# Kernel tuning notes

Measured on AMD Instinct MI355X. Metric: run time of the kernel, lower is better.

The kernel has to match this reference:

```python
import jax, jax.numpy as jnp
import numpy as np

CONF_THRESH = 0.3
NMS_THRESH = 0.5
TOP_K = 64
VAR = (0.1, 0.2)  # standard SSD decode variances


def setup_inputs() -> dict:
    key = jax.random.key(0)
    k1, k2, k3 = jax.random.split(key, 3)
    B, A, C = 16, 16384, 81
    loc = jax.random.normal(k1, (B, A, 4), jnp.float32)
    conf = jax.random.normal(k2, (B, A, C), jnp.float32)
    anchors = jax.random.uniform(k3, (A, 4), jnp.float32)  # cxcywh in [0,1]
    return {"loc": loc, "conf": conf, "anchors": anchors}


def _decode(loc, anchors):
    # SSD-style decode: loc [A,4] offsets, anchors [A,4] cxcywh -> corners [A,4]
    cxcy = anchors[:, :2] + loc[:, :2] * VAR[0] * anchors[:, 2:]
    wh = anchors[:, 2:] * jnp.exp(loc[:, 2:] * VAR[1])
    tl = cxcy - wh * 0.5
    return jnp.concatenate([tl, tl + wh], axis=1)


def _iou(box, boxes):
    # box [4], boxes [A,4] in corner format
    tl = jnp.maximum(box[:2], boxes[:, :2])
    br = jnp.minimum(box[2:], boxes[:, 2:])
    wh = jnp.clip(br - tl, 0.0)
    inter = wh[:, 0] * wh[:, 1]
    a1 = (box[2] - box[0]) * (box[3] - box[1])
    a2 = (boxes[:, 2] - boxes[:, 0]) * (boxes[:, 3] - boxes[:, 1])
    return inter / (a1 + a2 - inter)


def _nms(boxes, scores):
    # greedy NMS for one (batch, class) lane; boxes [A,4], scores [A]
    s0 = jnp.where(scores > CONF_THRESH, scores, -1.0)

    def step(s, _):
        i = jnp.argmax(s)
        sc = s[i]
        box = boxes[i]
        keep = sc > 0.0  # -1 means masked/suppressed; valid scores > conf_thresh > 0
        supp = jnp.where(_iou(box, boxes) > NMS_THRESH, -1.0, s).at[i].set(-1.0)
        s_next = jnp.where(keep, supp, s)
        row = jnp.where(keep, jnp.concatenate([sc[None], box]),
                        jnp.zeros((5,), s.dtype))
        return s_next, row

    _, rows = jax.lax.scan(step, s0, None, length=TOP_K)
    return rows  # [TOP_K, 5] = (score, x1, y1, x2, y2), zero-padded


def reference(loc, conf, anchors):
    conf = jax.nn.sigmoid(conf)                      # [B,A,C]
    boxes = jax.vmap(_decode, in_axes=(0, None))(loc, anchors)  # [B,A,4]
    scores = jnp.swapaxes(conf, 1, 2)                # [B,C,A]
    per_class = jax.vmap(_nms, in_axes=(None, 0))    # over classes
    out = jax.vmap(per_class)(boxes, scores)         # [B,C,TOP_K,5]
    return out
```

## Files before the change

### kernel.cpp

```cpp
#include <hip/hip_runtime.h>
#include <math.h>

constexpr int B_N  = 16;
constexpr int A_N  = 16384;
constexpr int C_N  = 81;
constexpr int TOPK = 64;
constexpr int DNT  = 256;
constexpr int NBINS = 232;
constexpr int CAP   = 512;
constexpr unsigned BIN_BASE = 0x3E99u;
constexpr int SNT = 256;
constexpr int BC_N = B_N * C_N;

constexpr int TA   = 64;
constexpr int TNT  = 256;
constexpr int TILE_ELEMS = TA * C_N;
constexpr int TILE_F4    = TILE_ELEMS / 4;

__global__ __launch_bounds__(DNT) void decode_kernel(const float4* __restrict__ loc,
                                                     const float4* __restrict__ anch,
                                                     float4* __restrict__ boxes) {
    int i = blockIdx.x * DNT + threadIdx.x;
    int a = i & (A_N - 1);
    float4 l  = loc[i];
    float4 an = anch[a];
    float cx = an.x + (l.x * 0.1f) * an.z;
    float cy = an.y + (l.y * 0.1f) * an.w;
    float w  = an.z * expf(l.z * 0.2f);
    float h  = an.w * expf(l.w * 0.2f);
    float x1 = cx - w * 0.5f;
    float y1 = cy - h * 0.5f;
    boxes[i] = make_float4(x1, y1, x1 + w, y1 + h);
}

__global__ __launch_bounds__(TNT) void sigT_kernel(const float* __restrict__ conf,
                                                   float* __restrict__ scoresT) {
    __shared__ float4 tile4[TILE_F4];
    float* tile = (float*)tile4;

    const int a0 = blockIdx.x * TA;
    const int b  = blockIdx.y;
    const int t  = threadIdx.x;

    const float4* src = (const float4*)(conf + ((size_t)b * A_N + a0) * C_N);
#pragma unroll
    for (int i = 0; i < (TILE_F4 + TNT - 1) / TNT; ++i) {
        int idx4 = i * TNT + t;
        if (idx4 < TILE_F4) {
            float4 x = src[idx4];
            float4 v;
            v.x = 1.0f / (1.0f + expf(-x.x));
            v.y = 1.0f / (1.0f + expf(-x.y));
            v.z = 1.0f / (1.0f + expf(-x.z));
            v.w = 1.0f / (1.0f + expf(-x.w));
            tile4[idx4] = v;
        }
    }
    __syncthreads();
    float* dst = scoresT + (size_t)b * C_N * A_N + a0;
#pragma unroll
    for (int i = 0; i < (TILE_F4 + TNT - 1) / TNT; ++i) {
        int idx4 = i * TNT + t;
        if (idx4 < TILE_F4) {
            int cc  = idx4 >> 4;
            int al4 = idx4 & 15;
            int e   = al4 * 4 * C_N + cc;
            float4 v;
            v.x = tile[e];
            v.y = tile[e + C_N];
            v.z = tile[e + 2 * C_N];
            v.w = tile[e + 3 * C_N];
            ((float4*)(dst + (size_t)cc * A_N))[al4] = v;
        }
    }
}

__device__ __forceinline__ void sort_gather_scan64(
        unsigned long long* cand, float4* cbox, int C, int lane,
        const float4* __restrict__ bptr, float* __restrict__ optr,
        float& rx1, float& ry1, float& rx2, float& ry2, float& rar,
        int& acc, int& kout) {
    unsigned long long key[8];
#pragma unroll
    for (int r = 0; r < 8; ++r) {
        int sidx = r * 64 + lane;
        key[r] = (sidx < C) ? cand[sidx] : 0ull;
    }
#pragma unroll
    for (int k = 2; k <= CAP; k <<= 1) {
#pragma unroll
        for (int j = k >> 1; j > 0; j >>= 1) {
            if (j >= 64) {
                int jr = j >> 6;
#pragma unroll
                for (int r = 0; r < 8; ++r) {
                    int rp = r ^ jr;
                    if (rp > r) {
                        int e = r * 64 + lane;
                        bool up = ((e & k) == 0);
                        unsigned long long va = key[r], vb = key[rp];
                        bool sw = up ? (va < vb) : (va > vb);
                        if (sw) { key[r] = vb; key[rp] = va; }
                    }
                }
            } else {
#pragma unroll
                for (int r = 0; r < 8; ++r) {
                    int e = r * 64 + lane;
                    bool up    = ((e & k) == 0);
                    bool isLow = ((lane & j) == 0);
                    unsigned long long va = key[r];
                    unsigned long long vb = __shfl_xor(va, j, 64);
                    bool keepMax = (up == isLow);
                    key[r] = keepMax ? (va > vb ? va : vb) : (va < vb ? va : vb);
                }
            }
        }
    }
    __syncthreads();
#pragma unroll
    for (int r = 0; r < 8; ++r) cand[r * 64 + lane] = key[r];
    __syncthreads();
#pragma unroll
    for (int r = 0; r < 8; ++r) {
        int e = r * 64 + lane;
        if (e < C) cbox[e] = bptr[(int)(~(unsigned)cand[e])];
    }
    __syncthreads();

    int ts = 0;
    unsigned long long k0 = cand[0];
    float4 cb = cbox[0];
    while (ts < C) {
        unsigned long long nk = 0ull;
        float4 nb = cb;
        if (ts + 1 < C) { nk = cand[ts + 1]; nb = cbox[ts + 1]; }
        float sc = __uint_as_float((unsigned)(k0 >> 32));
        float ca = (cb.z - cb.x) * (cb.w - cb.y);
        bool over = false;
        if (lane < acc) {
            float tlx = fmaxf(rx1, cb.x);
            float tly = fmaxf(ry1, cb.y);
            float brx = fminf(rx2, cb.z);
            float bry = fminf(ry2, cb.w);
            float iw  = fmaxf(brx - tlx, 0.0f);
            float ih  = fmaxf(bry - tly, 0.0f);
            float inter = iw * ih;
            float iou = inter / (rar + ca - inter);
            over = iou > 0.5f;
        }
        if (!__any(over)) {
            if (lane == acc) { rx1 = cb.x; ry1 = cb.y; rx2 = cb.z; ry2 = cb.w; rar = ca; }
            if (lane == 0) {
                float* o = optr + (size_t)kout * 5;
                o[0] = sc; o[1] = cb.x; o[2] = cb.y; o[3] = cb.z; o[4] = cb.w;
            }
            acc++; kout++;
            if (acc == TOPK) break;
        }
        ++ts; k0 = nk; cb = nb;
    }
}

__global__ __launch_bounds__(SNT) void select_kernel(
        const float* __restrict__ scoresT,
        unsigned long long* __restrict__ g_cand,
        int* __restrict__ g_hist,
        int* __restrict__ g_cnt,
        int* __restrict__ g_blo) {
    __shared__ int hist[NBINS];
    __shared__ int s_cnt;

    const int bc = blockIdx.x;
    const int t  = threadIdx.x;

    for (int i = t; i < NBINS; i += SNT) hist[i] = 0;
    if (t == 0) s_cnt = 0;
    __syncthreads();

    const float4* sptr = (const float4*)(scoresT + (size_t)bc * A_N);

    for (int i = 0; i < A_N / 4 / SNT; ++i) {
        float4 s4 = sptr[t + SNT * i];
        float s[4] = {s4.x, s4.y, s4.z, s4.w};
#pragma unroll
        for (int q = 0; q < 4; ++q) {
            if (s[q] > 0.3f) {
                unsigned u = __float_as_uint(s[q]);
                int bin = (int)(u >> 16) - (int)BIN_BASE;
                bin = bin < 0 ? 0 : (bin > NBINS - 1 ? NBINS - 1 : bin);
                atomicAdd(&hist[bin], 1);
            }
        }
    }
    __syncthreads();

    for (int i = t; i < NBINS; i += SNT) g_hist[bc * NBINS + i] = hist[i];

    int lo = NBINS, tot = 0;
    while (lo > 0) {
        int cnt = hist[lo - 1];
        if (tot + cnt > CAP) {
            if (tot == 0) { lo--; }
            break;
        }
        tot += cnt; lo--;
    }
    const int bin_lo = lo;

    if (bin_lo < NBINS) {
        for (int i = 0; i < A_N / 4 / SNT; ++i) {
            float4 s4 = sptr[t + SNT * i];
            float s[4] = {s4.x, s4.y, s4.z, s4.w};
#pragma unroll
            for (int q = 0; q < 4; ++q) {
                if (s[q] > 0.3f) {
                    unsigned u = __float_as_uint(s[q]);
                    int bin = (int)(u >> 16) - (int)BIN_BASE;
                    bin = bin < 0 ? 0 : (bin > NBINS - 1 ? NBINS - 1 : bin);
                    if (bin >= bin_lo && bin < NBINS) {
                        int slot = atomicAdd(&s_cnt, 1);
                        if (slot < CAP) {
                            unsigned a = (unsigned)(4 * (t + SNT * i) + q);
                            g_cand[(size_t)bc * CAP + slot] =
                                ((unsigned long long)u << 32) | (unsigned)(~a);
                        }
                    }
                }
            }
        }
    }
    __syncthreads();
    if (t == 0) {
        int C = s_cnt; if (C > CAP) C = CAP;
        g_cnt[bc] = C;
        g_blo[bc] = bin_lo;
    }
}

__global__ __launch_bounds__(64, 4) void nms_sorted_kernel(
        const float* __restrict__ scoresT,
        const float4* __restrict__ boxes,
        const unsigned long long* __restrict__ g_cand,
        const int* __restrict__ g_hist,
        const int* __restrict__ g_cnt,
        const int* __restrict__ g_blo,
        float* __restrict__ out) {
    __shared__ int hist[NBINS];
    __shared__ unsigned long long cand[CAP];
    __shared__ float4 cbox[CAP];
    __shared__ int s_cnt;

    const int bc   = blockIdx.x;
    const int b    = bc / C_N;
    const int lane = threadIdx.x;

    const float4* sptr = (const float4*)(scoresT + (size_t)bc * A_N);
    const float4* bptr = boxes + (size_t)b * A_N;
    float* optr = out + (size_t)bc * TOPK * 5;

    for (int i = lane; i < NBINS; i += 64) hist[i] = g_hist[bc * NBINS + i];
    const int C0 = g_cnt[bc];
    int bin_hi   = g_blo[bc];
    for (int e = lane; e < C0; e += 64) cand[e] = g_cand[(size_t)bc * CAP + e];
    __syncthreads();

    float rx1 = 0.f, ry1 = 0.f, rx2 = 0.f, ry2 = 0.f, rar = 0.f;
    int acc = 0, kout = 0;

    if (C0 > 0)
        sort_gather_scan64(cand, cbox, C0, lane, bptr, optr,
                           rx1, ry1, rx2, ry2, rar, acc, kout);

    while (acc < TOPK) {
        int lo = bin_hi, tot = 0;
        while (lo > 0) {
            int cnt = hist[lo - 1];
            if (tot + cnt > CAP) {
                if (tot == 0) { lo--; }
                break;
            }
            tot += cnt; lo--;
        }
        const int bin_lo = lo;
        if (bin_lo == bin_hi) break;
        if (lane == 0) s_cnt = 0;
        __syncthreads();

        for (int i = 0; i < A_N / 4 / 64; ++i) {
            float4 s4 = sptr[lane + 64 * i];
            float s[4] = {s4.x, s4.y, s4.z, s4.w};
#pragma unroll
            for (int q = 0; q < 4; ++q) {
                if (s[q] > 0.3f) {
                    unsigned u = __float_as_uint(s[q]);
                    int bin = (int)(u >> 16) - (int)BIN_BASE;
                    bin = bin < 0 ? 0 : (bin > NBINS - 1 ? NBINS - 1 : bin);
                    if (bin >= bin_lo && bin < bin_hi) {
                        int slot = atomicAdd(&s_cnt, 1);
                        if (slot < CAP) {
                            unsigned a = (unsigned)(4 * (lane + 64 * i) + q);
                            cand[slot] = ((unsigned long long)u << 32) | (unsigned)(~a);
                        }
                    }
                }
            }
        }
        __syncthreads();
        int C = s_cnt; if (C > CAP) C = CAP;
        if (C > 0)
            sort_gather_scan64(cand, cbox, C, lane, bptr, optr,
                               rx1, ry1, rx2, ry2, rar, acc, kout);
        bin_hi = bin_lo;
    }

    {
        float* o  = optr + (size_t)kout * 5;
        int   rem = (TOPK - kout) * 5;
        for (int i = lane; i < rem; i += 64) o[i] = 0.0f;
    }
}

__global__ __launch_bounds__(SNT, 4) void select_nms_fused(
        const float* __restrict__ scoresT,
        const float4* __restrict__ boxes,
        float* __restrict__ out) {
    __shared__ int hist[NBINS];
    __shared__ unsigned long long cand[CAP];
    __shared__ float4 cbox[CAP];
    __shared__ int s_cnt, s_acc, s_kout;

    const int bc   = blockIdx.x;
    const int b    = bc / C_N;
    const int t    = threadIdx.x;
    const int lane = t & 63;
    const int wv   = t >> 6;

    for (int i = t; i < NBINS; i += SNT) hist[i] = 0;
    if (t == 0) { s_acc = 0; s_kout = 0; }
    __syncthreads();

    const float4* sptr = (const float4*)(scoresT + (size_t)bc * A_N);
    const float4* bptr = boxes + (size_t)b * A_N;
    float* optr = out + (size_t)bc * TOPK * 5;

    for (int i = 0; i < A_N / 4 / SNT; ++i) {
        float4 s4 = sptr[t + SNT * i];
        float s[4] = {s4.x, s4.y, s4.z, s4.w};
#pragma unroll
        for (int q = 0; q < 4; ++q) {
            if (s[q] > 0.3f) {
                unsigned u = __float_as_uint(s[q]);
                int bin = (int)(u >> 16) - (int)BIN_BASE;
                bin = bin < 0 ? 0 : (bin > NBINS - 1 ? NBINS - 1 : bin);
                atomicAdd(&hist[bin], 1);
            }
        }
    }
    __syncthreads();

    float rx1 = 0.f, ry1 = 0.f, rx2 = 0.f, ry2 = 0.f, rar = 0.f;
    int acc = 0, kout = 0;

    int bin_hi = NBINS;
    for (;;) {
        int lo = bin_hi, tot = 0;
        while (lo > 0) {
            int cnt = hist[lo - 1];
            if (tot + cnt > CAP) { if (tot == 0) { lo--; } break; }
            tot += cnt; lo--;
        }
        const int bin_lo = lo;
        if (bin_lo == bin_hi) break;
        if (t == 0) s_cnt = 0;
        __syncthreads();

        for (int i = 0; i < A_N / 4 / SNT; ++i) {
            float4 s4 = sptr[t + SNT * i];
            float s[4] = {s4.x, s4.y, s4.z, s4.w};
#pragma unroll
            for (int q = 0; q < 4; ++q) {
                if (s[q] > 0.3f) {
                    unsigned u = __float_as_uint(s[q]);
                    int bin = (int)(u >> 16) - (int)BIN_BASE;
                    bin = bin < 0 ? 0 : (bin > NBINS - 1 ? NBINS - 1 : bin);
                    if (bin >= bin_lo && bin < bin_hi) {
                        int slot = atomicAdd(&s_cnt, 1);
                        if (slot < CAP) {
                            unsigned a = (unsigned)(4 * (t + SNT * i) + q);
                            cand[slot] = ((unsigned long long)u << 32) | (unsigned)(~a);
                        }
                    }
                }
            }
        }
        __syncthreads();
        int C = s_cnt; if (C > CAP) C = CAP;

        if (C > 0) {
            if (wv == 0) {
                unsigned long long key[8];
#pragma unroll
                for (int r = 0; r < 8; ++r) {
                    int sidx = r * 64 + lane;
                    key[r] = (sidx < C) ? cand[sidx] : 0ull;
                }
#pragma unroll
                for (int k = 2; k <= CAP; k <<= 1) {
#pragma unroll
                    for (int j = k >> 1; j > 0; j >>= 1) {
                        if (j >= 64) {
                            int jr = j >> 6;
#pragma unroll
                            for (int r = 0; r < 8; ++r) {
                                int rp = r ^ jr;
                                if (rp > r) {
                                    int e = r * 64 + lane;
                                    bool up = ((e & k) == 0);
                                    unsigned long long va = key[r], vb = key[rp];
                                    bool sw = up ? (va < vb) : (va > vb);
                                    if (sw) { key[r] = vb; key[rp] = va; }
                                }
                            }
                        } else {
#pragma unroll
                            for (int r = 0; r < 8; ++r) {
                                int e = r * 64 + lane;
                                bool up    = ((e & k) == 0);
                                bool isLow = ((lane & j) == 0);
                                unsigned long long va = key[r];
                                unsigned long long vb = __shfl_xor(va, j, 64);
                                bool keepMax = (up == isLow);
                                key[r] = keepMax ? (va > vb ? va : vb)
                                                 : (va < vb ? va : vb);
                            }
                        }
                    }
                }
#pragma unroll
                for (int r = 0; r < 8; ++r) cand[r * 64 + lane] = key[r];
            }
            __syncthreads();

            for (int e = t; e < CAP; e += SNT)
                if (e < C) cbox[e] = bptr[(int)(~(unsigned)cand[e])];
            __syncthreads();

            if (wv == 0) {
                int ts = 0;
                unsigned long long k0 = cand[0];
                float4 cb = cbox[0];
                while (ts < C) {
                    unsigned long long nk = 0ull;
                    float4 nb = cb;
                    if (ts + 1 < C) { nk = cand[ts + 1]; nb = cbox[ts + 1]; }
                    float sc = __uint_as_float((unsigned)(k0 >> 32));
                    float ca = (cb.z - cb.x) * (cb.w - cb.y);
                    bool over = false;
                    if (lane < acc) {
                        float tlx = fmaxf(rx1, cb.x);
                        float tly = fmaxf(ry1, cb.y);
                        float brx = fminf(rx2, cb.z);
                        float bry = fminf(ry2, cb.w);
                        float iw  = fmaxf(brx - tlx, 0.0f);
                        float ih  = fmaxf(bry - tly, 0.0f);
                        float inter = iw * ih;
                        float iou = inter / (rar + ca - inter);
                        over = iou > 0.5f;
                    }
                    if (!__any(over)) {
                        if (lane == acc) { rx1 = cb.x; ry1 = cb.y; rx2 = cb.z; ry2 = cb.w; rar = ca; }
                        if (lane == 0) {
                            float* o = optr + (size_t)kout * 5;
                            o[0] = sc; o[1] = cb.x; o[2] = cb.y; o[3] = cb.z; o[4] = cb.w;
                        }
                        acc++; kout++;
                        if (acc == TOPK) break;
                    }
                    ++ts; k0 = nk; cb = nb;
                }
                if (lane == 0) { s_acc = acc; s_kout = kout; }
            }
            __syncthreads();
            if (s_acc >= TOPK) break;
        }
        bin_hi = bin_lo;
    }

    {
        const int ko = s_kout;
        float* o  = optr + (size_t)ko * 5;
        int   rem = (TOPK - ko) * 5;
        for (int i = t; i < rem; i += SNT) o[i] = 0.0f;
    }
}

__global__ __launch_bounds__(64, 4) void nms_fallback(const float* __restrict__ conf,
                                                      const float4* __restrict__ boxes,
                                                      float* __restrict__ out) {
    __shared__ int hist[NBINS];
    __shared__ unsigned long long cand[CAP];
    __shared__ float4 cbox[CAP];
    __shared__ int s_cnt;

    const int c    = blockIdx.x;
    const int b    = blockIdx.y;
    const int lane = threadIdx.x;

    const float4* bptr = boxes + (size_t)b * A_N;
    const float*  cptr = conf + (size_t)b * A_N * C_N + c;
    float* optr = out + (size_t)(b * C_N + c) * TOPK * 5;

    for (int i = lane; i < NBINS; i += 64) hist[i] = 0;
    __syncthreads();
    for (int i = 0; i < A_N / 256; ++i) {
        int a0 = 4 * (lane + 64 * i);
#pragma unroll
        for (int q = 0; q < 4; ++q) {
            float x = cptr[(size_t)(a0 + q) * C_N];
            float s = 1.0f / (1.0f + expf(-x));
            if (s > 0.3f) {
                unsigned u = __float_as_uint(s);
                int bin = (int)(u >> 16) - (int)BIN_BASE;
                bin = bin < 0 ? 0 : (bin > NBINS - 1 ? NBINS - 1 : bin);
                atomicAdd(&hist[bin], 1);
            }
        }
    }
    __syncthreads();

    float rx1 = 0.f, ry1 = 0.f, rx2 = 0.f, ry2 = 0.f, rar = 0.f;
    int acc = 0, kout = 0;
    int bin_hi = NBINS;
    for (;;) {
        int lo = bin_hi, tot = 0;
        while (lo > 0) {
            int cnt = hist[lo - 1];
            if (tot + cnt > CAP) { if (tot == 0) { lo--; } break; }
            tot += cnt; lo--;
        }
        const int bin_lo = lo;
        if (bin_lo == bin_hi) break;
        if (lane == 0) s_cnt = 0;
        __syncthreads();
        for (int i = 0; i < A_N / 256; ++i) {
            int a0 = 4 * (lane + 64 * i);
#pragma unroll
            for (int q = 0; q < 4; ++q) {
                float x = cptr[(size_t)(a0 + q) * C_N];
                float s = 1.0f / (1.0f + expf(-x));
                if (s > 0.3f) {
                    unsigned u = __float_as_uint(s);
                    int bin = (int)(u >> 16) - (int)BIN_BASE;
                    bin = bin < 0 ? 0 : (bin > NBINS - 1 ? NBINS - 1 : bin);
                    if (bin >= bin_lo && bin < bin_hi) {
                        int slot = atomicAdd(&s_cnt, 1);
                        if (slot < CAP)
                            cand[slot] = ((unsigned long long)u << 32) | (unsigned)(~(unsigned)(a0 + q));
                    }
                }
            }
        }
        __syncthreads();
        int C = s_cnt; if (C > CAP) C = CAP;
        if (C > 0)
            sort_gather_scan64(cand, cbox, C, lane, bptr, optr,
                               rx1, ry1, rx2, ry2, rar, acc, kout);
        if (acc == TOPK) break;
        bin_hi = bin_lo;
    }
    {
        float* o  = optr + (size_t)kout * 5;
        int   rem = (TOPK - kout) * 5;
        for (int i = lane; i < rem; i += 64) o[i] = 0.0f;
    }
}

extern "C" void kernel_launch(void* const* d_in, const int* in_sizes, int n_in,
                              void* d_out, int out_size, void* d_ws, size_t ws_size,
                              hipStream_t stream) {
    const float* loc     = (const float*)d_in[0];
    const float* conf    = (const float*)d_in[1];
    const float* anchors = (const float*)d_in[2];
    float* out = (float*)d_out;

    const size_t boxes_bytes  = (size_t)B_N * A_N * sizeof(float4);
    const size_t scores_bytes = (size_t)B_N * C_N * A_N * sizeof(float);
    const size_t cand_bytes   = (size_t)BC_N * CAP * sizeof(unsigned long long);
    const size_t hist_bytes   = (size_t)BC_N * NBINS * sizeof(int);
    const size_t cnt_bytes    = (size_t)BC_N * sizeof(int);
    const size_t full_bytes   = boxes_bytes + scores_bytes + cand_bytes +
                                hist_bytes + 2 * cnt_bytes;

    float4* boxes = (float4*)d_ws;

    decode_kernel<<<(B_N * A_N) / DNT, DNT, 0, stream>>>(
        (const float4*)loc, (const float4*)anchors, boxes);

    if (ws_size >= full_bytes) {
        char* p = (char*)d_ws + boxes_bytes;
        float* scoresT = (float*)p;                 p += scores_bytes;
        unsigned long long* g_cand = (unsigned long long*)p; p += cand_bytes;
        int* g_hist = (int*)p;                      p += hist_bytes;
        int* g_cnt  = (int*)p;                      p += cnt_bytes;
        int* g_blo  = (int*)p;

        sigT_kernel<<<dim3(A_N / TA, B_N), TNT, 0, stream>>>(conf, scoresT);
        select_kernel<<<dim3(BC_N), SNT, 0, stream>>>(scoresT, g_cand, g_hist, g_cnt, g_blo);
        nms_sorted_kernel<<<dim3(BC_N), 64, 0, stream>>>(scoresT, boxes, g_cand,
                                                         g_hist, g_cnt, g_blo, out);
    } else if (ws_size >= boxes_bytes + scores_bytes) {
        float* scoresT = (float*)((char*)d_ws + boxes_bytes);
        sigT_kernel<<<dim3(A_N / TA, B_N), TNT, 0, stream>>>(conf, scoresT);
        select_nms_fused<<<dim3(BC_N), SNT, 0, stream>>>(scoresT, boxes, out);
    } else {
        nms_fallback<<<dim3(C_N, B_N), 64, 0, stream>>>(conf, boxes, out);
    }
}
```

Measured before the change: 221.7 us.

## Replace sequential candidate scan with register bitonic sort and parallel suppression

Adds process_band64, which sorts each band of up to 512 candidates with a register-resident bitonic network using wave shuffles. It then does greedy NMS by having each accepted box suppress all register-held candidates in parallel through an alive bitmask and ballot. This replaces the earlier scan, which tested every candidate against the accepted boxes one at a time (one lane per accepted box, with __any). Accepted boxes are kept in shared memory so later bands can be pre-suppressed. It costs more registers, so launch bounds drop from 4 to 2 blocks per SM.

```diff
diff --git a/kernel.cpp b/kernel.cpp
--- a/kernel.cpp
+++ b/kernel.cpp
@@ -162,6 +162,118 @@
     }
 }
 
+__device__ __forceinline__ void suppress_pass(
+        unsigned& aliveM, const float4& bb, float bar,
+        const float4 (&breg)[8], const float (&careg)[8]) {
+#pragma unroll
+    for (int r = 0; r < 8; ++r) {
+        float tlx = fmaxf(bb.x, breg[r].x);
+        float tly = fmaxf(bb.y, breg[r].y);
+        float brx = fminf(bb.z, breg[r].z);
+        float bry = fminf(bb.w, breg[r].w);
+        float iw  = fmaxf(brx - tlx, 0.0f);
+        float ih  = fmaxf(bry - tly, 0.0f);
+        float inter = iw * ih;
+        float iou = inter / (bar + careg[r] - inter);
+        if (iou > 0.5f) aliveM &= ~(1u << r);
+    }
+}
+
+__device__ __forceinline__ void process_band64(
+        unsigned long long* cand, float4* cbox, float4* abox, float* aar,
+        int C, int lane,
+        const float4* __restrict__ bptr, float* __restrict__ optr,
+        int& acc, int& kout) {
+    unsigned long long key[8];
+#pragma unroll
+    for (int r = 0; r < 8; ++r) {
+        int sidx = r * 64 + lane;
+        key[r] = (sidx < C) ? cand[sidx] : 0ull;
+    }
+#pragma unroll
+    for (int k = 2; k <= CAP; k <<= 1) {
+#pragma unroll
+        for (int j = k >> 1; j > 0; j >>= 1) {
+            if (j >= 64) {
+                int jr = j >> 6;
+#pragma unroll
+                for (int r = 0; r < 8; ++r) {
+                    int rp = r ^ jr;
+                    if (rp > r) {
+                        int e = r * 64 + lane;
+                        bool up = ((e & k) == 0);
+                        unsigned long long va = key[r], vb = key[rp];
+                        bool sw = up ? (va < vb) : (va > vb);
+                        if (sw) { key[r] = vb; key[rp] = va; }
+                    }
+                }
+            } else {
+#pragma unroll
+                for (int r = 0; r < 8; ++r) {
+                    int e = r * 64 + lane;
+                    bool up    = ((e & k) == 0);
+                    bool isLow = ((lane & j) == 0);
+                    unsigned long long va = key[r];
+                    unsigned long long vb = __shfl_xor(va, j, 64);
+                    bool keepMax = (up == isLow);
+                    key[r] = keepMax ? (va > vb ? va : vb) : (va < vb ? va : vb);
+                }
+            }
+        }
+    }
+    __syncthreads();
+#pragma unroll
+    for (int r = 0; r < 8; ++r) cand[r * 64 + lane] = key[r];
+    __syncthreads();
+
+    float4 breg[8];
+    float  careg[8];
+#pragma unroll
+    for (int r = 0; r < 8; ++r) {
+        int e = r * 64 + lane;
+        float4 v = make_float4(0.f, 0.f, 0.f, 0.f);
+        if (e < C) { v = bptr[(int)(~(unsigned)cand[e])]; cbox[e] = v; }
+        breg[r]  = v;
+        careg[r] = (v.z - v.x) * (v.w - v.y);
+    }
+    __syncthreads();
+
+    unsigned aliveM = 0;
+#pragma unroll
+    for (int r = 0; r < 8; ++r)
+        if (r * 64 + lane < C) aliveM |= (1u << r);
+
+    for (int a = 0; a < acc; ++a) {
+        float4 bb = abox[a];
+        float bar = aar[a];
+        suppress_pass(aliveM, bb, bar, breg, careg);
+    }
+
+    int rStart = 0;
+    while (acc < TOPK) {
+        int estar = -1;
+        for (int r = rStart; r < 8; ++r) {
+            unsigned long long m = __ballot((aliveM >> r) & 1);
+            if (m != 0ull) { estar = r * 64 + __builtin_ctzll(m); rStart = r; break; }
+        }
+        if (estar < 0) break;
+
+        unsigned long long k0 = cand[estar];
+        float4 bb = cbox[estar];
+        float sc  = __uint_as_float((unsigned)(k0 >> 32));
+        float bar = (bb.z - bb.x) * (bb.w - bb.y);
+
+        if (lane == 0) {
+            float* o = optr + (size_t)kout * 5;
+            o[0] = sc; o[1] = bb.x; o[2] = bb.y; o[3] = bb.z; o[4] = bb.w;
+            abox[acc] = bb; aar[acc] = bar;
+        }
+        acc++; kout++;
+
+        suppress_pass(aliveM, bb, bar, breg, careg);
+    }
+}
+
 __global__ __launch_bounds__(SNT) void select_kernel(
         const float* __restrict__ scoresT,
         unsigned long long* __restrict__ g_cand,
@@ -238,7 +350,7 @@
     }
 }
 
-__global__ __launch_bounds__(64, 4) void nms_sorted_kernel(
+__global__ __launch_bounds__(64, 2) void nms_sorted_kernel(
         const float* __restrict__ scoresT,
         const float4* __restrict__ boxes,
         const unsigned long long* __restrict__ g_cand,
@@ -249,6 +361,8 @@
     __shared__ int hist[NBINS];
     __shared__ unsigned long long cand[CAP];
     __shared__ float4 cbox[CAP];
+    __shared__ float4 abox[TOPK];
+    __shared__ float  aar[TOPK];
     __shared__ int s_cnt;
 
     const int bc   = blockIdx.x;
@@ -265,12 +379,10 @@
     for (int e = lane; e < C0; e += 64) cand[e] = g_cand[(size_t)bc * CAP + e];
     __syncthreads();
 
-    float rx1 = 0.f, ry1 = 0.f, rx2 = 0.f, ry2 = 0.f, rar = 0.f;
     int acc = 0, kout = 0;
 
     if (C0 > 0)
-        sort_gather_scan64(cand, cbox, C0, lane, bptr, optr,
-                           rx1, ry1, rx2, ry2, rar, acc, kout);
+        process_band64(cand, cbox, abox, aar, C0, lane, bptr, optr, acc, kout);
 
     while (acc < TOPK) {
         int lo = bin_hi, tot = 0;
@@ -309,8 +421,7 @@
         __syncthreads();
         int C = s_cnt; if (C > CAP) C = CAP;
         if (C > 0)
-            sort_gather_scan64(cand, cbox, C, lane, bptr, optr,
-                               rx1, ry1, rx2, ry2, rar, acc, kout);
+            process_band64(cand, cbox, abox, aar, C, lane, bptr, optr, acc, kout);
         bin_hi = bin_lo;
     }
 
```

Measured after the change: 254.8 us. +14.9%, slower.

## Replace sort-then-scan NMS with register-resident iterative argmax suppression

Applied to the files above, without the earlier changes.

The per-(batch,class) NMS kernel no longer sorts each candidate band in shared memory and scans it. Each lane now holds up to 8 candidate keys and boxes in registers, picks the winner each step with a wave-wide shuffle max, and suppresses overlapping keys in parallel. Boxes accepted from earlier bands are kept in shared memory and applied to new bands first. This removes the sort and the sequential per-candidate wave votes, at the cost of more registers (launch bounds lowered to 2 waves) and up to 64 argmax reductions per band.

```diff
diff --git a/kernel.cpp b/kernel.cpp
--- a/kernel.cpp
+++ b/kernel.cpp
@@ -162,6 +162,76 @@
     }
 }
 
+__device__ __forceinline__ void suppress_keys(
+        unsigned long long (&key)[8],
+        const float4 (&breg)[8], const float (&careg)[8],
+        const float4& bb, float bar) {
+#pragma unroll
+    for (int r = 0; r < 8; ++r) {
+        float tlx = fmaxf(bb.x, breg[r].x);
+        float tly = fmaxf(bb.y, breg[r].y);
+        float brx = fminf(bb.z, breg[r].z);
+        float bry = fminf(bb.w, breg[r].w);
+        float iw  = fmaxf(brx - tlx, 0.0f);
+        float ih  = fmaxf(bry - tly, 0.0f);
+        float inter = iw * ih;
+        float iou = inter / (bar + careg[r] - inter);
+        if (iou > 0.5f) key[r] = 0ull;
+    }
+}
+
+__device__ __forceinline__ void process_band_argmax(
+        unsigned long long (&key)[8], int C, int lane,
+        const float4* __restrict__ bptr, float* __restrict__ optr,
+        float4* abox, float* aar, int& acc, int& kout) {
+    float4 breg[8];
+    float  careg[8];
+#pragma unroll
+    for (int r = 0; r < 8; ++r) {
+        int e = r * 64 + lane;
+        float4 v = make_float4(0.f, 0.f, 0.f, 0.f);
+        if (e < C) v = bptr[(int)(~(unsigned)key[r])];
+        else       key[r] = 0ull;
+        breg[r]  = v;
+        careg[r] = (v.z - v.x) * (v.w - v.y);
+    }
+
+    for (int a = 0; a < acc; ++a) {
+        float4 bb = abox[a];
+        float  ba = aar[a];
+        suppress_keys(key, breg, careg, bb, ba);
+    }
+
+    while (acc < TOPK) {
+        unsigned long long bk = 0ull;
+#pragma unroll
+        for (int r = 0; r < 8; ++r)
+            if (key[r] > bk) bk = key[r];
+        unsigned long long gk = bk;
+#pragma unroll
+        for (int j = 1; j < 64; j <<= 1) {
+            unsigned long long o = __shfl_xor(gk, j, 64);
+            if (o > gk) gk = o;
+        }
+        if (gk == 0ull) break;
+
+        unsigned hi  = (unsigned)(gk >> 32);
+        int aidx = (int)__builtin_amdgcn_readfirstlane((int)(~(unsigned)gk));
+        float4 wb = bptr[aidx];
+        float war = (wb.z - wb.x) * (wb.w - wb.y);
+
+        if (lane == 0) {
+            float* o = optr + (size_t)kout * 5;
+            o[0] = __uint_as_float(hi);
+            o[1] = wb.x; o[2] = wb.y; o[3] = wb.z; o[4] = wb.w;
+            abox[acc] = wb; aar[acc] = war;
+        }
+        acc++; kout++;
+
+        suppress_keys(key, breg, careg, wb, war);
+    }
+}
+
 __global__ __launch_bounds__(SNT) void select_kernel(
         const float* __restrict__ scoresT,
         unsigned long long* __restrict__ g_cand,
@@ -238,7 +308,7 @@
     }
 }
 
-__global__ __launch_bounds__(64, 4) void nms_sorted_kernel(
+__global__ __launch_bounds__(64, 2) void nms_argmax_kernel(
         const float* __restrict__ scoresT,
         const float4* __restrict__ boxes,
         const unsigned long long* __restrict__ g_cand,
@@ -248,7 +318,8 @@
         float* __restrict__ out) {
     __shared__ int hist[NBINS];
     __shared__ unsigned long long cand[CAP];
-    __shared__ float4 cbox[CAP];
+    __shared__ float4 abox[TOPK];
+    __shared__ float  aar[TOPK];
     __shared__ int s_cnt;
 
     const int bc   = blockIdx.x;
@@ -262,15 +333,18 @@
     for (int i = lane; i < NBINS; i += 64) hist[i] = g_hist[bc * NBINS + i];
     const int C0 = g_cnt[bc];
     int bin_hi   = g_blo[bc];
-    for (int e = lane; e < C0; e += 64) cand[e] = g_cand[(size_t)bc * CAP + e];
-    __syncthreads();
-
-    float rx1 = 0.f, ry1 = 0.f, rx2 = 0.f, ry2 = 0.f, rar = 0.f;
+
     int acc = 0, kout = 0;
 
-    if (C0 > 0)
-        sort_gather_scan64(cand, cbox, C0, lane, bptr, optr,
-                           rx1, ry1, rx2, ry2, rar, acc, kout);
+    if (C0 > 0) {
+        unsigned long long key[8];
+#pragma unroll
+        for (int r = 0; r < 8; ++r) {
+            int e = r * 64 + lane;
+            key[r] = (e < C0) ? g_cand[(size_t)bc * CAP + e] : 0ull;
+        }
+        process_band_argmax(key, C0, lane, bptr, optr, abox, aar, acc, kout);
+    }
 
     while (acc < TOPK) {
         int lo = bin_hi, tot = 0;
@@ -308,9 +382,15 @@
         }
         __syncthreads();
         int C = s_cnt; if (C > CAP) C = CAP;
-        if (C > 0)
-            sort_gather_scan64(cand, cbox, C, lane, bptr, optr,
-                               rx1, ry1, rx2, ry2, rar, acc, kout);
+        if (C > 0) {
+            unsigned long long key[8];
+#pragma unroll
+            for (int r = 0; r < 8; ++r) {
+                int e = r * 64 + lane;
+                key[r] = (e < C) ? cand[e] : 0ull;
+            }
+            process_band_argmax(key, C, lane, bptr, optr, abox, aar, acc, kout);
+        }
         bin_hi = bin_lo;
     }
 
@@ -607,7 +687,7 @@
 
         sigT_kernel<<<dim3(A_N / TA, B_N), TNT, 0, stream>>>(conf, scoresT);
         select_kernel<<<dim3(BC_N), SNT, 0, stream>>>(scoresT, g_cand, g_hist, g_cnt, g_blo);
-        nms_sorted_kernel<<<dim3(BC_N), 64, 0, stream>>>(scoresT, boxes, g_cand,
+        nms_argmax_kernel<<<dim3(BC_N), 64, 0, stream>>>(scoresT, boxes, g_cand,
                                                          g_hist, g_cnt, g_blo, out);
     } else if (ws_size >= boxes_bytes + scores_bytes) {
         float* scoresT = (float*)((char*)d_ws + boxes_bytes);
```

Result: slower. 290.1 us (+30.8%).
